# Optimization experiments

Measured on AMD Instinct MI355X. Metric: run time of the kernel, lower is better.

Reference implementation:

```python
import jax, jax.numpy as jnp
import numpy as np


def setup_inputs() -> dict:
    key = jax.random.key(0)
    kq, kk, kv, km = jax.random.split(key, 4)
    b, h, s, d = 4, 16, 2048, 64
    q = jax.random.normal(kq, (b, h, s, d), dtype=jnp.float32)
    k = jax.random.normal(kk, (b, h, s, d), dtype=jnp.float32)
    v = jax.random.normal(kv, (b, h, s, d), dtype=jnp.float32)
    # True = attend (keep), False = masked out (matches torch semantics where
    # ~attention_mask marks positions to fill with -min)
    attention_mask = jax.random.randint(km, (b, s), 0, 2).astype(jnp.bool_)
    return {"q": q, "k": k, "v": v, "attention_mask": attention_mask}


def reference(q, k, v, attention_mask):
    # scaled dot-product attention: softmax(q k^T / sqrt(d)) v
    scale = q.shape[-1] ** (-0.5)
    sim = jnp.einsum("bhid,bhjd->bhij", q, k) * scale  # (b,h,s,s)
    neg = jnp.finfo(sim.dtype).min
    # mask broadcast (b,1,1,s): keep where True, fill with finfo.min where False
    sim = jnp.where(attention_mask[:, None, None, :], sim, neg)
    attn = jax.nn.softmax(sim, axis=-1)
    return jnp.einsum("bhij,bhjd->bhid", attn, v)
```

## Files before the change

kernel.cpp:

```cpp
#include <hip/hip_runtime.h>
#include <hip/hip_bf16.h>

typedef __attribute__((ext_vector_type(8))) short short8;
typedef __attribute__((ext_vector_type(4))) float floatx4;

constexpr int B = 4, H = 16, S = 2048, D = 64;
constexpr int BM = 64;
constexpr int BN = 64;
constexpr int LDK = 72;
constexpr int LDP = 72;

#define QSCALE (0.125f * 1.44269504088896f)

__device__ __forceinline__ short8 ld8f_bf(const float* p, float sc) {
  floatx4 a = *(const floatx4*)p;
  floatx4 b = *(const floatx4*)(p + 4);
  union { short8 s; __hip_bfloat162 h[4]; } u;
  u.h[0] = __float22bfloat162_rn(make_float2(a[0] * sc, a[1] * sc));
  u.h[1] = __float22bfloat162_rn(make_float2(a[2] * sc, a[3] * sc));
  u.h[2] = __float22bfloat162_rn(make_float2(b[0] * sc, b[1] * sc));
  u.h[3] = __float22bfloat162_rn(make_float2(b[2] * sc, b[3] * sc));
  return u.s;
}

__device__ __forceinline__ unsigned pk2(float lo, float hi) {
  __hip_bfloat162 h = __float22bfloat162_rn(make_float2(lo, hi));
  return *reinterpret_cast<unsigned*>(&h);
}

__global__ __launch_bounds__(256, 2)
void attn_flash_kernel(const float* __restrict__ Q, const float* __restrict__ Kp,
                       const float* __restrict__ Vp, const int* __restrict__ Mask,
                       float* __restrict__ Out) {
  __shared__ __align__(16) short ks[2][BN * LDK];
  __shared__ __align__(16) short vs[2][D * 64];
  __shared__ __align__(16) short ps[4][16 * LDP];
  __shared__ __align__(16) int ms[2][BN];

  const int t = threadIdx.x;
  const int wave = t >> 6;
  const int lane = t & 63;
  const int quad = lane >> 4;
  const int lm = lane & 15;

  const int bh = blockIdx.y;
  const int bb = bh >> 4;
  const int mblk = blockIdx.x;

  const float* Qb = Q + (size_t)bh * S * D;
  const float* Kb = Kp + (size_t)bh * S * D;
  const float* Vb = Vp + (size_t)bh * S * D;
  const int* Mb = Mask + bb * S;

  const int qrow = mblk * BM + wave * 16 + lm;
  const float* qp = Qb + (size_t)qrow * D;
  const short8 qf0 = ld8f_bf(qp + 0 * 32 + quad * 8, QSCALE);
  const short8 qf1 = ld8f_bf(qp + 1 * 32 + quad * 8, QSCALE);

  short8 ones;
#pragma unroll
  for (int j = 0; j < 8; ++j) ones[j] = (short)0x3F80;

  floatx4 acc[4], accl;
#pragma unroll
  for (int d = 0; d < 4; ++d) acc[d] = (floatx4){0.f, 0.f, 0.f, 0.f};
  accl = (floatx4){0.f, 0.f, 0.f, 0.f};

  const int r0 = t >> 3;
  const int c0 = t & 7;
  const int r1 = r0 + 32;
  const int kp = t & 31;
  const int cv = t >> 5;
  const float* kg0 = Kb + (size_t)r0 * D + c0 * 8;
  const float* kg1 = Kb + (size_t)r1 * D + c0 * 8;
  const float* vg0 = Vb + (size_t)(2 * kp) * D + cv * 8;
  const float* vg1 = Vb + (size_t)(2 * kp + 1) * D + cv * 8;

  floatx4 kr[2][2], vr[2][2];
  int mreg = 0;

  auto stage_load = [&](int kb) {
    const size_t off = (size_t)kb * D;
    kr[0][0] = *(const floatx4*)(kg0 + off);
    kr[0][1] = *(const floatx4*)(kg0 + off + 4);
    kr[1][0] = *(const floatx4*)(kg1 + off);
    kr[1][1] = *(const floatx4*)(kg1 + off + 4);
    vr[0][0] = *(const floatx4*)(vg0 + off);
    vr[0][1] = *(const floatx4*)(vg0 + off + 4);
    vr[1][0] = *(const floatx4*)(vg1 + off);
    vr[1][1] = *(const floatx4*)(vg1 + off + 4);
    if (t < BN) mreg = Mb[kb + t];
  };

  auto stage_write = [&](int buf) {
    if (t < BN) ms[buf][t] = mreg;
#pragma unroll
    for (int it = 0; it < 2; ++it) {
      const int r = it ? r1 : r0;
      floatx4 a = kr[it][0], b = kr[it][1];
      union { short8 s; __hip_bfloat162 h[4]; } u;
      u.h[0] = __float22bfloat162_rn(make_float2(a[0], a[1]));
      u.h[1] = __float22bfloat162_rn(make_float2(a[2], a[3]));
      u.h[2] = __float22bfloat162_rn(make_float2(b[0], b[1]));
      u.h[3] = __float22bfloat162_rn(make_float2(b[2], b[3]));
      *(short8*)&ks[buf][r * LDK + c0 * 8] = u.s;
    }
#pragma unroll
    for (int j = 0; j < 4; ++j) {
      *(unsigned*)&vs[buf][(cv * 8 + j) * 64 + ((2 * kp) ^ (j << 3))] =
          pk2(vr[0][0][j], vr[1][0][j]);
      *(unsigned*)&vs[buf][(cv * 8 + 4 + j) * 64 + ((2 * kp) ^ ((4 + j) << 3))] =
          pk2(vr[0][1][j], vr[1][1][j]);
    }
  };

  stage_load(0);
  stage_write(0);

  int cur = 0;
  for (int kb = 0; kb < S; kb += BN) {
    __syncthreads();
    const bool hn = (kb + BN) < S;
    if (hn) stage_load(kb + BN);

    const short* ksc = ks[cur];
    const short* vsc = vs[cur];
    const int* msc = ms[cur];

    floatx4 sc[4];
    __builtin_amdgcn_s_setprio(1);
#pragma unroll
    for (int nt = 0; nt < 4; ++nt) {
      short8 kf0 = *(const short8*)&ksc[(nt * 16 + lm) * LDK + 0 * 32 + quad * 8];
      short8 kf1 = *(const short8*)&ksc[(nt * 16 + lm) * LDK + 1 * 32 + quad * 8];
      floatx4 z = (floatx4){0.f, 0.f, 0.f, 0.f};
      z = __builtin_amdgcn_mfma_f32_16x16x32_bf16(kf0, qf0, z, 0, 0, 0);
      z = __builtin_amdgcn_mfma_f32_16x16x32_bf16(kf1, qf1, z, 0, 0, 0);
      sc[nt] = z;
    }
    __builtin_amdgcn_s_setprio(0);

    float s_el[4][4];
#pragma unroll
    for (int nt = 0; nt < 4; ++nt) {
      int4 mm = *(const int4*)&msc[nt * 16 + quad * 4];
      int mv[4] = {mm.x, mm.y, mm.z, mm.w};
#pragma unroll
      for (int r = 0; r < 4; ++r)
        s_el[nt][r] = mv[r] ? __builtin_exp2f(sc[nt][r]) : 0.0f;
    }

    short* pw = &ps[wave][0];
#pragma unroll
    for (int nt = 0; nt < 4; ++nt) {
      uint2 pp = make_uint2(pk2(s_el[nt][0], s_el[nt][1]),
                            pk2(s_el[nt][2], s_el[nt][3]));
      *(uint2*)&pw[lm * LDP + nt * 16 + quad * 4] = pp;
    }

    __builtin_amdgcn_s_setprio(1);
    const int vswz = (lm & 7) << 3;
#pragma unroll
    for (int kt = 0; kt < 2; ++kt) {
      short8 af = *(const short8*)&pw[lm * LDP + kt * 32 + quad * 8];
      accl = __builtin_amdgcn_mfma_f32_16x16x32_bf16(af, ones, accl, 0, 0, 0);
#pragma unroll
      for (int dn = 0; dn < 4; ++dn) {
        short8 bf = *(const short8*)&vsc[(dn * 16 + lm) * 64 +
                                         ((kt * 32 + quad * 8) ^ vswz)];
        acc[dn] = __builtin_amdgcn_mfma_f32_16x16x32_bf16(af, bf, acc[dn], 0, 0, 0);
      }
    }
    __builtin_amdgcn_s_setprio(0);

    if (hn) stage_write(cur ^ 1);
    cur ^= 1;
  }

#pragma unroll
  for (int r = 0; r < 4; ++r) {
    float inv = 1.0f / accl[r];
    int row = mblk * BM + wave * 16 + quad * 4 + r;
    float* op = Out + (size_t)(bh * S + row) * D;
#pragma unroll
    for (int dn = 0; dn < 4; ++dn)
      op[dn * 16 + lm] = acc[dn][r] * inv;
  }
}

extern "C" void kernel_launch(void* const* d_in, const int* in_sizes, int n_in,
                              void* d_out, int out_size, void* d_ws, size_t ws_size,
                              hipStream_t stream) {
  const float* q = (const float*)d_in[0];
  const float* k = (const float*)d_in[1];
  const float* v = (const float*)d_in[2];
  const int* mask = (const int*)d_in[3];
  float* out = (float*)d_out;
  dim3 grid(S / BM, B * H);
  attn_flash_kernel<<<grid, dim3(256), 0, stream>>>(q, k, v, mask, out);
}
```

Measured before the change: 294.0 us.

## Switch to 32x32x16 MFMA, keep P in registers, double query tile

Replaces the 16x16x32 bf16 MFMAs with 32x32x16 MFMAs, with each wave owning 32 query rows, so the block tile grows to 128 rows. The score-to-P layout is chosen so the exp'd scores can be packed straight into A operands. This removes the per-wave LDS round trip for P, and the V LDS swizzle is adjusted to match. It aims to cut LDS traffic and K/V reloads per query row and to raise MFMA efficiency, at the cost of more accumulator registers, half as many blocks, and a higher occupancy target that may cause spills.

```diff
diff --git a/kernel.cpp b/kernel.cpp
--- a/kernel.cpp
+++ b/kernel.cpp
@@ -3,12 +3,12 @@
 
 typedef __attribute__((ext_vector_type(8))) short short8;
 typedef __attribute__((ext_vector_type(4))) float floatx4;
+typedef __attribute__((ext_vector_type(16))) float floatx16;
 
 constexpr int B = 4, H = 16, S = 2048, D = 64;
-constexpr int BM = 64;
+constexpr int BM = 128;
 constexpr int BN = 64;
 constexpr int LDK = 72;
-constexpr int LDP = 72;
 
 #define QSCALE (0.125f * 1.44269504088896f)
 
@@ -28,20 +28,19 @@
   return *reinterpret_cast<unsigned*>(&h);
 }
 
-__global__ __launch_bounds__(256, 2)
+__global__ __launch_bounds__(256, 3)
 void attn_flash_kernel(const float* __restrict__ Q, const float* __restrict__ Kp,
                        const float* __restrict__ Vp, const int* __restrict__ Mask,
                        float* __restrict__ Out) {
   __shared__ __align__(16) short ks[2][BN * LDK];
   __shared__ __align__(16) short vs[2][D * 64];
-  __shared__ __align__(16) short ps[4][16 * LDP];
   __shared__ __align__(16) int ms[2][BN];
 
   const int t = threadIdx.x;
   const int wave = t >> 6;
   const int lane = t & 63;
-  const int quad = lane >> 4;
-  const int lm = lane & 15;
+  const int l5 = lane & 31;
+  const int hi = lane >> 5;
 
   const int bh = blockIdx.y;
   const int bb = bh >> 4;
@@ -52,19 +51,24 @@
   const float* Vb = Vp + (size_t)bh * S * D;
   const int* Mb = Mask + bb * S;
 
-  const int qrow = mblk * BM + wave * 16 + lm;
+  const int qrow = mblk * BM + wave * 32 + l5;
   const float* qp = Qb + (size_t)qrow * D;
-  const short8 qf0 = ld8f_bf(qp + 0 * 32 + quad * 8, QSCALE);
-  const short8 qf1 = ld8f_bf(qp + 1 * 32 + quad * 8, QSCALE);
+  short8 qf[4];
+#pragma unroll
+  for (int kd = 0; kd < 4; ++kd)
+    qf[kd] = ld8f_bf(qp + kd * 16 + hi * 8, QSCALE);
 
   short8 ones;
 #pragma unroll
   for (int j = 0; j < 8; ++j) ones[j] = (short)0x3F80;
 
-  floatx4 acc[4], accl;
-#pragma unroll
-  for (int d = 0; d < 4; ++d) acc[d] = (floatx4){0.f, 0.f, 0.f, 0.f};
-  accl = (floatx4){0.f, 0.f, 0.f, 0.f};
+  floatx16 acc[2], accl;
+#pragma unroll
+  for (int d = 0; d < 2; ++d)
+#pragma unroll
+    for (int r = 0; r < 16; ++r) acc[d][r] = 0.f;
+#pragma unroll
+  for (int r = 0; r < 16; ++r) accl[r] = 0.f;
 
   const int r0 = t >> 3;
   const int c0 = t & 7;
@@ -75,6 +79,8 @@
   const float* kg1 = Kb + (size_t)r1 * D + c0 * 8;
   const float* vg0 = Vb + (size_t)(2 * kp) * D + cv * 8;
   const float* vg1 = Vb + (size_t)(2 * kp + 1) * D + cv * 8;
+  const int k2 = 2 * kp;
+  const int sk = (k2 & ~12) | ((k2 & 4) << 1) | ((k2 & 8) >> 1);
 
   floatx4 kr[2][2], vr[2][2];
   int mreg = 0;
@@ -107,9 +113,9 @@
     }
 #pragma unroll
     for (int j = 0; j < 4; ++j) {
-      *(unsigned*)&vs[buf][(cv * 8 + j) * 64 + ((2 * kp) ^ (j << 3))] =
+      *(unsigned*)&vs[buf][(cv * 8 + j) * 64 + (sk ^ (j << 3))] =
           pk2(vr[0][0][j], vr[1][0][j]);
-      *(unsigned*)&vs[buf][(cv * 8 + 4 + j) * 64 + ((2 * kp) ^ ((4 + j) << 3))] =
+      *(unsigned*)&vs[buf][(cv * 8 + 4 + j) * 64 + (sk ^ ((4 + j) << 3))] =
           pk2(vr[0][1][j], vr[1][1][j]);
     }
   };
@@ -127,48 +133,58 @@
     const short* vsc = vs[cur];
     const int* msc = ms[cur];
 
-    floatx4 sc[4];
+    floatx16 sc[2];
+#pragma unroll
+    for (int nt = 0; nt < 2; ++nt)
+#pragma unroll
+      for (int r = 0; r < 16; ++r) sc[nt][r] = 0.f;
     __builtin_amdgcn_s_setprio(1);
 #pragma unroll
-    for (int nt = 0; nt < 4; ++nt) {
-      short8 kf0 = *(const short8*)&ksc[(nt * 16 + lm) * LDK + 0 * 32 + quad * 8];
-      short8 kf1 = *(const short8*)&ksc[(nt * 16 + lm) * LDK + 1 * 32 + quad * 8];
-      floatx4 z = (floatx4){0.f, 0.f, 0.f, 0.f};
-      z = __builtin_amdgcn_mfma_f32_16x16x32_bf16(kf0, qf0, z, 0, 0, 0);
-      z = __builtin_amdgcn_mfma_f32_16x16x32_bf16(kf1, qf1, z, 0, 0, 0);
-      sc[nt] = z;
-    }
+    for (int nt = 0; nt < 2; ++nt)
+#pragma unroll
+      for (int kd = 0; kd < 4; ++kd) {
+        short8 kf = *(const short8*)&ksc[(nt * 32 + l5) * LDK + kd * 16 + hi * 8];
+        sc[nt] = __builtin_amdgcn_mfma_f32_32x32x16_bf16(kf, qf[kd], sc[nt], 0, 0, 0);
+      }
     __builtin_amdgcn_s_setprio(0);
 
-    float s_el[4][4];
-#pragma unroll
-    for (int nt = 0; nt < 4; ++nt) {
-      int4 mm = *(const int4*)&msc[nt * 16 + quad * 4];
-      int mv[4] = {mm.x, mm.y, mm.z, mm.w};
-#pragma unroll
-      for (int r = 0; r < 4; ++r)
-        s_el[nt][r] = mv[r] ? __builtin_exp2f(sc[nt][r]) : 0.0f;
-    }
-
-    short* pw = &ps[wave][0];
-#pragma unroll
-    for (int nt = 0; nt < 4; ++nt) {
-      uint2 pp = make_uint2(pk2(s_el[nt][0], s_el[nt][1]),
-                            pk2(s_el[nt][2], s_el[nt][3]));
-      *(uint2*)&pw[lm * LDP + nt * 16 + quad * 4] = pp;
-    }
+    float s_el[2][4][4];
+#pragma unroll
+    for (int nt = 0; nt < 2; ++nt)
+#pragma unroll
+      for (int g = 0; g < 4; ++g) {
+        int4 mm = *(const int4*)&msc[nt * 32 + 8 * g + 4 * hi];
+        int mv[4] = {mm.x, mm.y, mm.z, mm.w};
+#pragma unroll
+        for (int c = 0; c < 4; ++c)
+          s_el[nt][g][c] = mv[c] ? __builtin_exp2f(sc[nt][4 * g + c]) : 0.0f;
+      }
+
+    unsigned h[2][4][2];
+#pragma unroll
+    for (int nt = 0; nt < 2; ++nt)
+#pragma unroll
+      for (int g = 0; g < 4; ++g) {
+        h[nt][g][0] = pk2(s_el[nt][g][0], s_el[nt][g][1]);
+        h[nt][g][1] = pk2(s_el[nt][g][2], s_el[nt][g][3]);
+      }
 
     __builtin_amdgcn_s_setprio(1);
-    const int vswz = (lm & 7) << 3;
-#pragma unroll
-    for (int kt = 0; kt < 2; ++kt) {
-      short8 af = *(const short8*)&pw[lm * LDP + kt * 32 + quad * 8];
-      accl = __builtin_amdgcn_mfma_f32_16x16x32_bf16(af, ones, accl, 0, 0, 0);
-#pragma unroll
-      for (int dn = 0; dn < 4; ++dn) {
-        short8 bf = *(const short8*)&vsc[(dn * 16 + lm) * 64 +
-                                         ((kt * 32 + quad * 8) ^ vswz)];
-        acc[dn] = __builtin_amdgcn_mfma_f32_16x16x32_bf16(af, bf, acc[dn], 0, 0, 0);
+    const int vswz = (l5 & 7) << 3;
+#pragma unroll
+    for (int st = 0; st < 4; ++st) {
+      const int nt = st >> 1, a2 = (st & 1) * 2;
+      union { short8 s; unsigned u[4]; } af;
+      af.u[0] = h[nt][a2][0];
+      af.u[1] = h[nt][a2][1];
+      af.u[2] = h[nt][a2 + 1][0];
+      af.u[3] = h[nt][a2 + 1][1];
+      accl = __builtin_amdgcn_mfma_f32_32x32x16_bf16(af.s, ones, accl, 0, 0, 0);
+#pragma unroll
+      for (int dn = 0; dn < 2; ++dn) {
+        short8 bf = *(const short8*)&vsc[(dn * 32 + l5) * 64 +
+                                         ((st * 16 + hi * 8) ^ vswz)];
+        acc[dn] = __builtin_amdgcn_mfma_f32_32x32x16_bf16(af.s, bf, acc[dn], 0, 0, 0);
       }
     }
     __builtin_amdgcn_s_setprio(0);
@@ -178,13 +194,13 @@
   }
 
 #pragma unroll
-  for (int r = 0; r < 4; ++r) {
+  for (int r = 0; r < 16; ++r) {
     float inv = 1.0f / accl[r];
-    int row = mblk * BM + wave * 16 + quad * 4 + r;
+    int row = mblk * BM + wave * 32 + (r & 3) + 8 * (r >> 2) + 4 * hi;
     float* op = Out + (size_t)(bh * S + row) * D;
 #pragma unroll
-    for (int dn = 0; dn < 4; ++dn)
-      op[dn * 16 + lm] = acc[dn][r] * inv;
+    for (int dn = 0; dn < 2; ++dn)
+      op[dn * 32 + l5] = acc[dn][r] * inv;
   }
 }
 
```

Measured after the change: 507.3 us. 72.5% more time.

## Halve key tile to 32 and raise occupancy target to six blocks per CU

Applied to the files above, without the earlier changes.

Shrinks the key/value tile from 64 to 32 rows, cutting per-thread staging registers and shared memory, and raises the launch-bounds occupancy hint from 2 to 6 blocks. The V shared layout changes from an XOR swizzle to a padded stride of 40, and the per-thread load and store mapping is rebuilt to match. The goal is more resident waves to hide global load and exp latency. The cost is twice as many loop iterations and barriers per block, plus possible LDS bank conflicts from the padded layout.

```diff
diff --git a/kernel.cpp b/kernel.cpp
--- a/kernel.cpp
+++ b/kernel.cpp
@@ -6,9 +6,10 @@
 
 constexpr int B = 4, H = 16, S = 2048, D = 64;
 constexpr int BM = 64;
-constexpr int BN = 64;
+constexpr int BN = 32;
 constexpr int LDK = 72;
-constexpr int LDP = 72;
+constexpr int LDV = 40;
+constexpr int LDP = 40;
 
 #define QSCALE (0.125f * 1.44269504088896f)
 
@@ -28,12 +29,12 @@
   return *reinterpret_cast<unsigned*>(&h);
 }
 
-__global__ __launch_bounds__(256, 2)
+__global__ __launch_bounds__(256, 6)
 void attn_flash_kernel(const float* __restrict__ Q, const float* __restrict__ Kp,
                        const float* __restrict__ Vp, const int* __restrict__ Mask,
                        float* __restrict__ Out) {
   __shared__ __align__(16) short ks[2][BN * LDK];
-  __shared__ __align__(16) short vs[2][D * 64];
+  __shared__ __align__(16) short vs[2][D * LDV];
   __shared__ __align__(16) short ps[4][16 * LDP];
   __shared__ __align__(16) int ms[2][BN];
 
@@ -68,50 +69,35 @@
 
   const int r0 = t >> 3;
   const int c0 = t & 7;
-  const int r1 = r0 + 32;
-  const int kp = t & 31;
-  const int cv = t >> 5;
+  const int kp = t & 15;
+  const int cv = t >> 4;
   const float* kg0 = Kb + (size_t)r0 * D + c0 * 8;
-  const float* kg1 = Kb + (size_t)r1 * D + c0 * 8;
-  const float* vg0 = Vb + (size_t)(2 * kp) * D + cv * 8;
-  const float* vg1 = Vb + (size_t)(2 * kp + 1) * D + cv * 8;
+  const float* vg0 = Vb + (size_t)(2 * kp) * D + cv * 4;
+  const float* vg1 = Vb + (size_t)(2 * kp + 1) * D + cv * 4;
 
-  floatx4 kr[2][2], vr[2][2];
+  floatx4 kr0, kr1, vr0, vr1;
   int mreg = 0;
 
   auto stage_load = [&](int kb) {
     const size_t off = (size_t)kb * D;
-    kr[0][0] = *(const floatx4*)(kg0 + off);
-    kr[0][1] = *(const floatx4*)(kg0 + off + 4);
-    kr[1][0] = *(const floatx4*)(kg1 + off);
-    kr[1][1] = *(const floatx4*)(kg1 + off + 4);
-    vr[0][0] = *(const floatx4*)(vg0 + off);
-    vr[0][1] = *(const floatx4*)(vg0 + off + 4);
-    vr[1][0] = *(const floatx4*)(vg1 + off);
-    vr[1][1] = *(const floatx4*)(vg1 + off + 4);
+    kr0 = *(const floatx4*)(kg0 + off);
+    kr1 = *(const floatx4*)(kg0 + off + 4);
+    vr0 = *(const floatx4*)(vg0 + off);
+    vr1 = *(const floatx4*)(vg1 + off);
     if (t < BN) mreg = Mb[kb + t];
   };
 
   auto stage_write = [&](int buf) {
     if (t < BN) ms[buf][t] = mreg;
+    union { short8 s; __hip_bfloat162 h[4]; } u;
+    u.h[0] = __float22bfloat162_rn(make_float2(kr0[0], kr0[1]));
+    u.h[1] = __float22bfloat162_rn(make_float2(kr0[2], kr0[3]));
+    u.h[2] = __float22bfloat162_rn(make_float2(kr1[0], kr1[1]));
+    u.h[3] = __float22bfloat162_rn(make_float2(kr1[2], kr1[3]));
+    *(short8*)&ks[buf][r0 * LDK + c0 * 8] = u.s;
 #pragma unroll
-    for (int it = 0; it < 2; ++it) {
-      const int r = it ? r1 : r0;
-      floatx4 a = kr[it][0], b = kr[it][1];
-      union { short8 s; __hip_bfloat162 h[4]; } u;
-      u.h[0] = __float22bfloat162_rn(make_float2(a[0], a[1]));
-      u.h[1] = __float22bfloat162_rn(make_float2(a[2], a[3]));
-      u.h[2] = __float22bfloat162_rn(make_float2(b[0], b[1]));
-      u.h[3] = __float22bfloat162_rn(make_float2(b[2], b[3]));
-      *(short8*)&ks[buf][r * LDK + c0 * 8] = u.s;
-    }
-#pragma unroll
-    for (int j = 0; j < 4; ++j) {
-      *(unsigned*)&vs[buf][(cv * 8 + j) * 64 + ((2 * kp) ^ (j << 3))] =
-          pk2(vr[0][0][j], vr[1][0][j]);
-      *(unsigned*)&vs[buf][(cv * 8 + 4 + j) * 64 + ((2 * kp) ^ ((4 + j) << 3))] =
-          pk2(vr[0][1][j], vr[1][1][j]);
-    }
+    for (int j = 0; j < 4; ++j)
+      *(unsigned*)&vs[buf][(cv * 4 + j) * LDV + 2 * kp] = pk2(vr0[j], vr1[j]);
   };
 
   stage_load(0);
@@ -127,10 +113,10 @@
     const short* vsc = vs[cur];
     const int* msc = ms[cur];
 
-    floatx4 sc[4];
+    floatx4 sc[2];
     __builtin_amdgcn_s_setprio(1);
 #pragma unroll
-    for (int nt = 0; nt < 4; ++nt) {
+    for (int nt = 0; nt < 2; ++nt) {
       short8 kf0 = *(const short8*)&ksc[(nt * 16 + lm) * LDK + 0 * 32 + quad * 8];
       short8 kf1 = *(const short8*)&ksc[(nt * 16 + lm) * LDK + 1 * 32 + quad * 8];
       floatx4 z = (floatx4){0.f, 0.f, 0.f, 0.f};
@@ -140,36 +126,26 @@
     }
     __builtin_amdgcn_s_setprio(0);
 
-    float s_el[4][4];
+    short* pw = &ps[wave][0];
 #pragma unroll
-    for (int nt = 0; nt < 4; ++nt) {
+    for (int nt = 0; nt < 2; ++nt) {
       int4 mm = *(const int4*)&msc[nt * 16 + quad * 4];
       int mv[4] = {mm.x, mm.y, mm.z, mm.w};
-#pragma unroll
-      for (int r = 0; r < 4; ++r)
-        s_el[nt][r] = mv[r] ? __builtin_exp2f(sc[nt][r]) : 0.0f;
-    }
-
-    short* pw = &ps[wave][0];
-#pragma unroll
-    for (int nt = 0; nt < 4; ++nt) {
-      uint2 pp = make_uint2(pk2(s_el[nt][0], s_el[nt][1]),
-                            pk2(s_el[nt][2], s_el[nt][3]));
+      float s0 = mv[0] ? __builtin_exp2f(sc[nt][0]) : 0.0f;
+      float s1 = mv[1] ? __builtin_exp2f(sc[nt][1]) : 0.0f;
+      float s2 = mv[2] ? __builtin_exp2f(sc[nt][2]) : 0.0f;
+      float s3 = mv[3] ? __builtin_exp2f(sc[nt][3]) : 0.0f;
+      uint2 pp = make_uint2(pk2(s0, s1), pk2(s2, s3));
       *(uint2*)&pw[lm * LDP + nt * 16 + quad * 4] = pp;
     }
 
     __builtin_amdgcn_s_setprio(1);
-    const int vswz = (lm & 7) << 3;
+    short8 af = *(const short8*)&pw[lm * LDP + quad * 8];
+    accl = __builtin_amdgcn_mfma_f32_16x16x32_bf16(af, ones, accl, 0, 0, 0);
 #pragma unroll
-    for (int kt = 0; kt < 2; ++kt) {
-      short8 af = *(const short8*)&pw[lm * LDP + kt * 32 + quad * 8];
-      accl = __builtin_amdgcn_mfma_f32_16x16x32_bf16(af, ones, accl, 0, 0, 0);
-#pragma unroll
-      for (int dn = 0; dn < 4; ++dn) {
-        short8 bf = *(const short8*)&vsc[(dn * 16 + lm) * 64 +
-                                         ((kt * 32 + quad * 8) ^ vswz)];
-        acc[dn] = __builtin_amdgcn_mfma_f32_16x16x32_bf16(af, bf, acc[dn], 0, 0, 0);
-      }
+    for (int dn = 0; dn < 4; ++dn) {
+      short8 bf = *(const short8*)&vsc[(dn * 16 + lm) * LDV + quad * 8];
+      acc[dn] = __builtin_amdgcn_mfma_f32_16x16x32_bf16(af, bf, acc[dn], 0, 0, 0);
     }
     __builtin_amdgcn_s_setprio(0);
 
```

Result: slower. 347.5 us (+18.2%).

## Deepen K/V prefetch to two tiles ahead with register double-buffering

Applied to the files above, without the earlier changes.

Restructures the KV loop into a manually unrolled pair of iterations, using two sets of register staging buffers (A/B) so that global loads are issued two tiles ahead instead of one. This gives each global load more latency to hide behind the MFMA compute. __syncthreads is replaced by a custom barrier that only waits on LDS counters, so outstanding global loads no longer stall at the barrier. The cost is higher register pressure from the second set of staging registers, which may cause spills under the 2-block launch bound.

```diff
diff --git a/kernel.cpp b/kernel.cpp
--- a/kernel.cpp
+++ b/kernel.cpp
@@ -9,6 +9,7 @@
 constexpr int BN = 64;
 constexpr int LDK = 72;
 constexpr int LDP = 72;
+constexpr int NT = S / BN;
 
 #define QSCALE (0.125f * 1.44269504088896f)
 
@@ -28,6 +29,11 @@
   return *reinterpret_cast<unsigned*>(&h);
 }
 
+__device__ __forceinline__ void wg_barrier() {
+  asm volatile("s_waitcnt lgkmcnt(0)" ::: "memory");
+  __builtin_amdgcn_s_barrier();
+}
+
 __global__ __launch_bounds__(256, 2)
 void attn_flash_kernel(const float* __restrict__ Q, const float* __restrict__ Kp,
                        const float* __restrict__ Vp, const int* __restrict__ Mask,
@@ -75,58 +81,52 @@
   const float* kg1 = Kb + (size_t)r1 * D + c0 * 8;
   const float* vg0 = Vb + (size_t)(2 * kp) * D + cv * 8;
   const float* vg1 = Vb + (size_t)(2 * kp + 1) * D + cv * 8;
-
-  floatx4 kr[2][2], vr[2][2];
-  int mreg = 0;
-
-  auto stage_load = [&](int kb) {
-    const size_t off = (size_t)kb * D;
-    kr[0][0] = *(const floatx4*)(kg0 + off);
-    kr[0][1] = *(const floatx4*)(kg0 + off + 4);
-    kr[1][0] = *(const floatx4*)(kg1 + off);
-    kr[1][1] = *(const floatx4*)(kg1 + off + 4);
-    vr[0][0] = *(const floatx4*)(vg0 + off);
-    vr[0][1] = *(const floatx4*)(vg0 + off + 4);
-    vr[1][0] = *(const floatx4*)(vg1 + off);
-    vr[1][1] = *(const floatx4*)(vg1 + off + 4);
-    if (t < BN) mreg = Mb[kb + t];
-  };
-
-  auto stage_write = [&](int buf) {
-    if (t < BN) ms[buf][t] = mreg;
-#pragma unroll
-    for (int it = 0; it < 2; ++it) {
-      const int r = it ? r1 : r0;
-      floatx4 a = kr[it][0], b = kr[it][1];
-      union { short8 s; __hip_bfloat162 h[4]; } u;
-      u.h[0] = __float22bfloat162_rn(make_float2(a[0], a[1]));
-      u.h[1] = __float22bfloat162_rn(make_float2(a[2], a[3]));
-      u.h[2] = __float22bfloat162_rn(make_float2(b[0], b[1]));
-      u.h[3] = __float22bfloat162_rn(make_float2(b[2], b[3]));
-      *(short8*)&ks[buf][r * LDK + c0 * 8] = u.s;
-    }
-#pragma unroll
-    for (int j = 0; j < 4; ++j) {
-      *(unsigned*)&vs[buf][(cv * 8 + j) * 64 + ((2 * kp) ^ (j << 3))] =
-          pk2(vr[0][0][j], vr[1][0][j]);
-      *(unsigned*)&vs[buf][(cv * 8 + 4 + j) * 64 + ((2 * kp) ^ ((4 + j) << 3))] =
-          pk2(vr[0][1][j], vr[1][1][j]);
-    }
-  };
-
-  stage_load(0);
-  stage_write(0);
-
-  int cur = 0;
-  for (int kb = 0; kb < S; kb += BN) {
-    __syncthreads();
-    const bool hn = (kb + BN) < S;
-    if (hn) stage_load(kb + BN);
-
-    const short* ksc = ks[cur];
-    const short* vsc = vs[cur];
-    const int* msc = ms[cur];
-
+  const int k2 = 2 * kp;
+
+  floatx4 kA00, kA01, kA10, kA11, vA00, vA01, vA10, vA11; int mA;
+  floatx4 kB00, kB01, kB10, kB11, vB00, vB01, vB10, vB11; int mB;
+
+#define STAGE_LOAD(kb, S_) do {                                             \
+    const size_t off_ = (size_t)(kb) * D;                                   \
+    k##S_##00 = *(const floatx4*)(kg0 + off_);                              \
+    k##S_##01 = *(const floatx4*)(kg0 + off_ + 4);                          \
+    k##S_##10 = *(const floatx4*)(kg1 + off_);                              \
+    k##S_##11 = *(const floatx4*)(kg1 + off_ + 4);                          \
+    v##S_##00 = *(const floatx4*)(vg0 + off_);                              \
+    v##S_##01 = *(const floatx4*)(vg0 + off_ + 4);                          \
+    v##S_##10 = *(const floatx4*)(vg1 + off_);                              \
+    v##S_##11 = *(const floatx4*)(vg1 + off_ + 4);                          \
+    m##S_ = Mb[(kb) + (t & 63)];                                            \
+  } while (0)
+
+#define STAGE_WRITE(buf, S_) do {                                           \
+    if (t < BN) ms[buf][t] = m##S_;                                         \
+    {                                                                       \
+      union { short8 s; __hip_bfloat162 h[4]; } u_;                         \
+      u_.h[0] = __float22bfloat162_rn(make_float2(k##S_##00[0], k##S_##00[1])); \
+      u_.h[1] = __float22bfloat162_rn(make_float2(k##S_##00[2], k##S_##00[3])); \
+      u_.h[2] = __float22bfloat162_rn(make_float2(k##S_##01[0], k##S_##01[1])); \
+      u_.h[3] = __float22bfloat162_rn(make_float2(k##S_##01[2], k##S_##01[3])); \
+      *(short8*)&ks[buf][r0 * LDK + c0 * 8] = u_.s;                         \
+      u_.h[0] = __float22bfloat162_rn(make_float2(k##S_##10[0], k##S_##10[1])); \
+      u_.h[1] = __float22bfloat162_rn(make_float2(k##S_##10[2], k##S_##10[3])); \
+      u_.h[2] = __float22bfloat162_rn(make_float2(k##S_##11[0], k##S_##11[1])); \
+      u_.h[3] = __float22bfloat162_rn(make_float2(k##S_##11[2], k##S_##11[3])); \
+      *(short8*)&ks[buf][r1 * LDK + c0 * 8] = u_.s;                         \
+    }                                                                       \
+    _Pragma("unroll")                                                       \
+    for (int j = 0; j < 4; ++j) {                                           \
+      *(unsigned*)&vs[buf][(cv * 8 + j) * 64 + (k2 ^ (j << 3))] =           \
+          pk2(v##S_##00[j], v##S_##10[j]);                                  \
+      *(unsigned*)&vs[buf][(cv * 8 + 4 + j) * 64 + (k2 ^ ((4 + j) << 3))] = \
+          pk2(v##S_##01[j], v##S_##11[j]);                                  \
+    }                                                                       \
+  } while (0)
+
+  short* pw = &ps[wave][0];
+  const int vswz = (lm & 7) << 3;
+
+  auto compute = [&](const short* ksc, const short* vsc, const int* msc) {
     floatx4 sc[4];
     __builtin_amdgcn_s_setprio(1);
 #pragma unroll
@@ -140,26 +140,19 @@
     }
     __builtin_amdgcn_s_setprio(0);
 
-    float s_el[4][4];
 #pragma unroll
     for (int nt = 0; nt < 4; ++nt) {
       int4 mm = *(const int4*)&msc[nt * 16 + quad * 4];
       int mv[4] = {mm.x, mm.y, mm.z, mm.w};
-#pragma unroll
-      for (int r = 0; r < 4; ++r)
-        s_el[nt][r] = mv[r] ? __builtin_exp2f(sc[nt][r]) : 0.0f;
-    }
-
-    short* pw = &ps[wave][0];
-#pragma unroll
-    for (int nt = 0; nt < 4; ++nt) {
-      uint2 pp = make_uint2(pk2(s_el[nt][0], s_el[nt][1]),
-                            pk2(s_el[nt][2], s_el[nt][3]));
+      float s0 = mv[0] ? __builtin_exp2f(sc[nt][0]) : 0.0f;
+      float s1 = mv[1] ? __builtin_exp2f(sc[nt][1]) : 0.0f;
+      float s2 = mv[2] ? __builtin_exp2f(sc[nt][2]) : 0.0f;
+      float s3 = mv[3] ? __builtin_exp2f(sc[nt][3]) : 0.0f;
+      uint2 pp = make_uint2(pk2(s0, s1), pk2(s2, s3));
       *(uint2*)&pw[lm * LDP + nt * 16 + quad * 4] = pp;
     }
 
     __builtin_amdgcn_s_setprio(1);
-    const int vswz = (lm & 7) << 3;
 #pragma unroll
     for (int kt = 0; kt < 2; ++kt) {
       short8 af = *(const short8*)&pw[lm * LDP + kt * 32 + quad * 8];
@@ -172,9 +165,22 @@
       }
     }
     __builtin_amdgcn_s_setprio(0);
-
-    if (hn) stage_write(cur ^ 1);
-    cur ^= 1;
+  };
+
+  STAGE_LOAD(0, A);
+  STAGE_WRITE(0, A);
+  STAGE_LOAD(BN, A);
+
+#pragma unroll 1
+  for (int tt = 0; tt < NT; tt += 2) {
+    wg_barrier();
+    if (tt + 2 < NT) STAGE_LOAD((tt + 2) * BN, B);
+    compute(ks[0], vs[0], ms[0]);
+    STAGE_WRITE(1, A);
+    wg_barrier();
+    if (tt + 3 < NT) STAGE_LOAD((tt + 3) * BN, A);
+    compute(ks[1], vs[1], ms[1]);
+    if (tt + 2 < NT) STAGE_WRITE(0, B);
   }
 
 #pragma unroll
```

Result: no change. 293.3 us (-0.2%).
